# Kernel optimization log

Hardware: AMD Instinct MI355X
Metric: run time of the kernel (lower is better)

Reference implementation:

```python
import jax, jax.numpy as jnp
import numpy as np

V, E, H = 30000, 512, 512
MARGIN = 0.05


def _lstm(x, wih, whh, b):
    # x: [N,T,E]; torch LSTM gate order i,f,g,o; returns outputs [N,T,H]
    N = x.shape[0]
    Hh = whh.shape[1]
    xproj = jnp.swapaxes(x, 0, 1) @ wih.T + b  # [T,N,4H], input proj hoisted out of scan

    def step(carry, xp):
        h, c = carry
        g = xp + h @ whh.T
        i, f, gg, o = jnp.split(g, 4, axis=-1)
        c = jax.nn.sigmoid(f) * c + jax.nn.sigmoid(i) * jnp.tanh(gg)
        h = jax.nn.sigmoid(o) * jnp.tanh(c)
        return (h, c), h

    h0 = jnp.zeros((N, Hh), x.dtype)
    _, hs = jax.lax.scan(step, (h0, h0), xproj)
    return jnp.swapaxes(hs, 0, 1)


def _attn_pool(feat, lengths, aw, ab, sw, sb):
    # batched masked-softmax attention pooling (replaces per-sample python loop)
    T = feat.shape[1]
    s = (jnp.tanh(feat @ aw.T + ab) @ sw.T + sb)[..., 0]  # [N,T]
    mask = jnp.arange(T)[None, :] < lengths[:, None]
    w = jax.nn.softmax(jnp.where(mask, s, -1e30), axis=1)
    return jnp.einsum('nt,nth->nh', w, feat)  # [N,H]


def _cos(a, b, eps=1e-8):
    na = jnp.maximum(jnp.linalg.norm(a, axis=-1), eps)
    nb = jnp.maximum(jnp.linalg.norm(b, axis=-1), eps)
    return jnp.sum(a * b, axis=-1) / (na * nb)


def setup_inputs() -> dict:
    key = jax.random.key(0)
    ks = jax.random.split(key, 24)
    B, BL, T, TD = 32, 8, 128, 256
    d = {}
    d['tran'] = jax.random.randint(ks[0], (B, BL, T), 1, V)
    d['tran_len'] = jax.random.randint(ks[1], (B,), 1, T + 1)
    d['tran_block_len'] = jax.random.randint(ks[2], (B, BL), 1, T + 1)
    d['doc_anchor'] = jax.random.randint(ks[3], (B, TD), 1, V)
    d['doc_anchor_len'] = jax.random.randint(ks[4], (B,), 1, TD + 1)
    d['doc_neg'] = jax.random.randint(ks[5], (B, TD), 1, V)
    d['doc_neg_len'] = jax.random.randint(ks[6], (B,), 1, TD + 1)
    sc = 0.05
    emb = jax.random.normal(ks[7], (V, E), jnp.float32) * sc
    d['emb'] = emb.at[0].set(0.0)  # padding_idx=0
    d['tran_wih'] = jax.random.normal(ks[8], (4 * H, E), jnp.float32) * sc
    d['tran_whh'] = jax.random.normal(ks[9], (4 * H, H), jnp.float32) * sc
    d['tran_b'] = jax.random.normal(ks[10], (4 * H,), jnp.float32) * sc
    d['doc_wih'] = jax.random.normal(ks[11], (4 * H, E), jnp.float32) * sc
    d['doc_whh'] = jax.random.normal(ks[12], (4 * H, H), jnp.float32) * sc
    d['doc_b'] = jax.random.normal(ks[13], (4 * H,), jnp.float32) * sc
    d['tran_attn_w'] = jax.random.normal(ks[14], (H, H), jnp.float32) * sc
    d['tran_attn_b'] = jax.random.normal(ks[15], (H,), jnp.float32) * sc
    d['tran_s_w'] = jax.random.normal(ks[16], (1, H), jnp.float32) * sc
    d['tran_s_b'] = jax.random.normal(ks[17], (1,), jnp.float32) * sc
    d['doc_attn_w'] = jax.random.normal(ks[18], (H, H), jnp.float32) * sc
    d['doc_attn_b'] = jax.random.normal(ks[19], (H,), jnp.float32) * sc
    d['doc_s_w'] = jax.random.normal(ks[20], (1, H), jnp.float32) * sc
    d['doc_s_b'] = jax.random.normal(ks[21], (1,), jnp.float32) * sc
    return d


def reference(tran, tran_len, tran_block_len, doc_anchor, doc_anchor_len,
              doc_neg, doc_neg_len, emb, tran_wih, tran_whh, tran_b,
              doc_wih, doc_whh, doc_b, tran_attn_w, tran_attn_b,
              tran_s_w, tran_s_b, doc_attn_w, doc_attn_b, doc_s_w, doc_s_b):
    B, BL, T = tran.shape
    # --- code side: encode B*BL sub-sequences, attn pool, tanh, max over block ---
    flat = tran.reshape(B * BL, T)
    feat = _lstm(emb[flat], tran_wih, tran_whh, tran_b)  # [B*BL,T,H]
    pooled = _attn_pool(feat, tran_block_len.reshape(-1),
                        tran_attn_w, tran_attn_b, tran_s_w, tran_s_b)
    pooled = jnp.tanh(pooled)  # use_tanh on attn output (tran path)
    code_repr = jnp.max(pooled.reshape(B, BL, H), axis=1)  # max_pool over block

    # --- doc side: attn pool, no trailing tanh (doc_encoding has no use_tanh branch) ---
    def doc_enc(tok, lens):
        f = _lstm(emb[tok], doc_wih, doc_whh, doc_b)
        return _attn_pool(f, lens, doc_attn_w, doc_attn_b, doc_s_w, doc_s_b)

    da = doc_enc(doc_anchor, doc_anchor_len)
    dn = doc_enc(doc_neg, doc_neg_len)

    anchor_sim = _cos(code_repr, da)
    neg_sim = _cos(code_repr, dn)
    loss = jnp.mean(jnp.clip(MARGIN - anchor_sim + neg_sim, 1e-6, None))
    return loss
```

## Files before the change

### kernel.cpp

```cpp
#include <hip/hip_runtime.h>
#include <hip/hip_bf16.h>

#define NSEQ 320
#define NTRAN 256
#define TT 128
#define TDOC 256
#define EH 512
#define XR_TRAN (NTRAN*TT)
#define XROWS (XR_TRAN + 64*TDOC)
#define HSLOTS 6
#define FW 264

typedef __attribute__((ext_vector_type(8))) short bf16x8v;
typedef __attribute__((ext_vector_type(4))) float f32x4v;

__device__ __align__(16) unsigned short g_xb [(size_t)XROWS*EH];
__device__ __align__(16) unsigned short g_wbx[2*2048*512];
__device__ __align__(16) unsigned short g_w2b[2*5*512*512];
__device__ float g_xp[(size_t)XROWS*2048];
__device__ float g_h [HSLOTS*NSEQ*EH];
__device__ float g_sc[64*260];
__device__ float g_pool[NSEQ*EH];
__device__ float g_loss;
__device__ unsigned g_gflag[48*FW];
__device__ unsigned g_sflag[16*FW];
__device__ unsigned g_aprog[48];

__device__ __forceinline__ float sigm(float x) { return 1.0f / (1.0f + expf(-x)); }

__device__ __forceinline__ float ldg_sys(const float* p) {
  return __hip_atomic_load(p, __ATOMIC_RELAXED, __HIP_MEMORY_SCOPE_SYSTEM);
}
__device__ __forceinline__ void stg_sys(float* p, float v) {
  __hip_atomic_store(p, v, __ATOMIC_RELAXED, __HIP_MEMORY_SCOPE_SYSTEM);
}
__device__ __forceinline__ unsigned ldu(const unsigned* p) {
  return __hip_atomic_load(p, __ATOMIC_RELAXED, __HIP_MEMORY_SCOPE_AGENT);
}
__device__ __forceinline__ unsigned short f2b(float f) {
  __hip_bfloat16 h = __float2bfloat16(f);
  return *reinterpret_cast<unsigned short*>(&h);
}

__global__ __launch_bounds__(256) void init_state() {
  int i = blockIdx.x*256 + threadIdx.x;
  if (i < NSEQ*EH) g_h[5*NSEQ*EH + i] = 0.0f;
  if (i < 64*260) g_sc[i] = 0.0f;
  if (i < 48*FW) g_gflag[i] = ((i % FW) == 0) ? 4u : 0u;
  if (i < 16*FW) g_sflag[i] = 0u;
  if (i < 48) g_aprog[i] = 0u;
  if (i == 0) g_loss = 0.0f;
}

__global__ __launch_bounds__(256) void build_wbx(
    const float* __restrict__ wih_t, const float* __restrict__ wih_d) {
  int idx = blockIdx.x*256 + threadIdx.x;
  if (idx >= 2*2048*512) return;
  int p = idx / (2048*512); int rem = idx % (2048*512);
  const float* wih = p ? wih_d : wih_t;
  g_wbx[idx] = f2b(wih[rem]);
}

__global__ __launch_bounds__(256) void build_wt2(
    const float* __restrict__ whh_t, const float* __restrict__ whh_d,
    const float* __restrict__ aw_t,  const float* __restrict__ aw_d) {
  int idx = blockIdx.x*256 + threadIdx.x;
  if (idx >= 2*5*512*512) return;
  int p  = idx / (5*512*512); int rem = idx % (5*512*512);
  int cg = rem / (512*512);   int r2  = rem % (512*512);
  int k  = r2 >> 9;           int c   = r2 & 511;
  float v;
  if (cg < 4) {
    int r = (c >> 7)*512 + cg*128 + (c & 127);
    const float* whh = p ? whh_d : whh_t;
    v = whh[r*512 + k];
  } else {
    const float* aw = p ? aw_d : aw_t;
    v = aw[c*512 + k];
  }
  g_w2b[((size_t)(p*5 + cg)*512 + k)*512 + c] = f2b(v);
}

__global__ __launch_bounds__(128) void pregather(
    const int* __restrict__ tran, const int* __restrict__ da_tok,
    const int* __restrict__ dn_tok, const float* __restrict__ emb) {
  int row = blockIdx.x;
  int tok;
  if (row < XR_TRAN) tok = tran[row];
  else {
    int q = row - XR_TRAN;
    tok = (q < 32*TDOC) ? da_tok[q] : dn_tok[q - 32*TDOC];
  }
  const float4* src = (const float4*)&emb[(size_t)tok*EH];
  float4 v = src[threadIdx.x];
  uint2 o;
  o.x = (unsigned)f2b(v.x) | ((unsigned)f2b(v.y) << 16);
  o.y = (unsigned)f2b(v.z) | ((unsigned)f2b(v.w) << 16);
  ((uint2*)&g_xb[(size_t)row*EH])[threadIdx.x] = o;
}

__global__ __launch_bounds__(512, 2) void xproj_mfma(
    const float* __restrict__ b_t, const float* __restrict__ b_d) {
  __shared__ short As[2][256*32];
  __shared__ short Bs[2][256*32];
  const int bid = blockIdx.x;
  const int mt = bid >> 3, ntb = bid & 7;
  const size_t mb = (size_t)mt * 256; const int nb = ntb * 256;
  const bool tp = (mb < XR_TRAN);
  const size_t wboff = (tp ? 0 : (size_t)2048*512);
  const float* __restrict__ bias = tp ? b_t : b_d;
  const int tid = threadIdx.x;
  const int l = tid & 63, w = tid >> 6;
  const int mw = w >> 2, nw = w & 3;

  f32x4v acc[8][4];
  #pragma unroll
  for (int m2 = 0; m2 < 8; ++m2)
    #pragma unroll
    for (int n2 = 0; n2 < 4; ++n2) acc[m2][n2] = (f32x4v){0.f, 0.f, 0.f, 0.f};

  uint4 rA[2], rB[2];
  auto stage_load = [&](int k0) {
    #pragma unroll
    for (int i = 0; i < 2; ++i) {
      int u = i*512 + tid;
      rA[i] = *(const uint4*)&g_xb[(mb + (u >> 2))*512 + k0 + (u & 3)*8];
      rB[i] = *(const uint4*)&g_wbx[wboff + (size_t)(nb + (u >> 2))*512 + k0 + (u & 3)*8];
    }
  };
  auto stage_write = [&](int buf) {
    #pragma unroll
    for (int i = 0; i < 2; ++i) {
      int u = i*512 + tid;
      *(uint4*)&As[buf][u*8] = rA[i];
      *(uint4*)&Bs[buf][u*8] = rB[i];
    }
  };

  stage_load(0); stage_write(0); __syncthreads();
  for (int ks = 0; ks < 16; ++ks) {
    const int buf = ks & 1;
    if (ks < 15) stage_load((ks + 1)*32);
    bf16x8v aF[8], bF[4];
    #pragma unroll
    for (int m2 = 0; m2 < 8; ++m2)
      aF[m2] = *(const bf16x8v*)&As[buf][(mw*128 + m2*16 + (l & 15))*32 + (l >> 4)*8];
    #pragma unroll
    for (int n2 = 0; n2 < 4; ++n2)
      bF[n2] = *(const bf16x8v*)&Bs[buf][(nw*64 + n2*16 + (l & 15))*32 + (l >> 4)*8];
    #pragma unroll
    for (int m2 = 0; m2 < 8; ++m2)
      #pragma unroll
      for (int n2 = 0; n2 < 4; ++n2)
        acc[m2][n2] = __builtin_amdgcn_mfma_f32_16x16x32_bf16(aF[m2], bF[n2], acc[m2][n2], 0, 0, 0);
    __syncthreads();
    if (ks < 15) stage_write(buf ^ 1);
    __syncthreads();
  }

  #pragma unroll
  for (int n2 = 0; n2 < 4; ++n2) {
    const int colg = nb + nw*64 + n2*16 + (l & 15);
    const int col2 = ((colg & 511) >> 7)*512 + (colg >> 9)*128 + (colg & 127);
    const float bv = bias[colg];
    #pragma unroll
    for (int m2 = 0; m2 < 8; ++m2) {
      #pragma unroll
      for (int r = 0; r < 4; ++r) {
        size_t row = mb + mw*128 + m2*16 + (l >> 4)*4 + r;
        g_xp[row*2048 + col2] = acc[m2][n2][r] + bv;
      }
    }
  }
}

template<int S, int CPL>
__device__ __forceinline__ void gemm2(const unsigned short* __restrict__ wsl,
                                      const float* __restrict__ ht,
                                      float* __restrict__ part,
                                      int kq, int lane) {
  constexpr int PW = CPL*64 + 4;
  float acc[CPL][S];
  #pragma unroll
  for (int c = 0; c < CPL; ++c)
    #pragma unroll
    for (int s = 0; s < S; ++s) acc[c][s] = 0.0f;
  const unsigned short* wp = wsl + (size_t)(kq*64)*512 + CPL*lane;
  const float* hb = ht + kq*64;
  #pragma unroll 2
  for (int k4 = 0; k4 < 16; ++k4) {
    float4 hv[S];
    #pragma unroll
    for (int s = 0; s < S; ++s) hv[s] = *(const float4*)&hb[s*516 + k4*4];
    #pragma unroll
    for (int i4 = 0; i4 < 4; ++i4) {
      float wf[CPL];
      if constexpr (CPL == 8) {
        uint4 wv = *(const uint4*)(wp + (size_t)(k4*4 + i4)*512);
        wf[0] = __uint_as_float(wv.x << 16); wf[1] = __uint_as_float(wv.x & 0xFFFF0000u);
        wf[2] = __uint_as_float(wv.y << 16); wf[3] = __uint_as_float(wv.y & 0xFFFF0000u);
        wf[4] = __uint_as_float(wv.z << 16); wf[5] = __uint_as_float(wv.z & 0xFFFF0000u);
        wf[6] = __uint_as_float(wv.w << 16); wf[7] = __uint_as_float(wv.w & 0xFFFF0000u);
      } else {
        uint2 wv = *(const uint2*)(wp + (size_t)(k4*4 + i4)*512);
        wf[0] = __uint_as_float(wv.x << 16); wf[1] = __uint_as_float(wv.x & 0xFFFF0000u);
        wf[2] = __uint_as_float(wv.y << 16); wf[3] = __uint_as_float(wv.y & 0xFFFF0000u);
      }
      #pragma unroll
      for (int s = 0; s < S; ++s) {
        float h = ((const float*)&hv[s])[i4];
        #pragma unroll
        for (int c = 0; c < CPL; ++c) acc[c][s] = fmaf(wf[c], h, acc[c][s]);
      }
    }
  }
  if (kq < 4) {
    #pragma unroll
    for (int s = 0; s < S; ++s)
      #pragma unroll
      for (int c = 0; c < CPL; ++c)
        part[(size_t)(kq*S + s)*PW + CPL*lane + c] = acc[c][s];
  }
  __syncthreads();
  if (kq >= 4) {
    const int q = kq - 4;
    #pragma unroll
    for (int s = 0; s < S; ++s)
      #pragma unroll
      for (int c = 0; c < CPL; ++c)
        part[(size_t)(q*S + s)*PW + CPL*lane + c] += acc[c][s];
  }
}

__global__ __launch_bounds__(512, 2) void persist(
    const int* __restrict__ tbl, const int* __restrict__ dal, const int* __restrict__ dnl,
    const float* __restrict__ ab_t, const float* __restrict__ ab_d,
    const float* __restrict__ sw_t, const float* __restrict__ sw_d,
    const float* __restrict__ sb_t, const float* __restrict__ sb_d) {
  __shared__ float sm[28920];
  float* part = sm;
  float* ht   = sm + 16512;
  float* cb   = sm + 20640;
  float* scr  = sm + 24736;
  float* ml   = sm + 24752;
  float* lenb = sm + 24768;
  float* alb  = sm + 24776;
  float* htB  = sm + 24792;

  const int b = blockIdx.x, tid = threadIdx.x;
  const int x = b & 7, m = b >> 3;
  bool tran; int cg, nt;
  if (x < 5) { tran = true; cg = x; nt = m; }
  else { int slot = (x - 5)*32 + m; tran = false; cg = slot >> 4; nt = slot & 15; }
  const int S     = tran ? 8 : 4;
  const int Ts    = tran ? TT : TDOC;
  const int sbase = tran ? nt*8 : NTRAN + nt*4;
  const bool isattn = (cg >= 4);
  const int gr = tran ? nt : 32 + nt;
  const unsigned AK = tran ? 1u : 2u;
  const int colbase = tran ? 0 : (cg - 4) * 256;
  const int wslice  = isattn ? 4 : cg;
  const unsigned short* __restrict__ wsl =
      g_w2b + (size_t)((tran ? 0 : 5) + wslice)*512*512 + (isattn ? colbase : 0);
  const float* __restrict__ ab  = tran ? ab_t : ab_d;
  const float* __restrict__ sw  = tran ? sw_t : sw_d;
  const float  sb = tran ? sb_t[0] : sb_d[0];

  for (int i = tid; i < 4096; i += 512) cb[i] = 0.0f;
  if (tid < S) {
    ml[tid*2] = -3.0e38f; ml[tid*2+1] = 0.0f;
    int s = sbase + tid;
    int len = tran ? tbl[s] : (s < NTRAN+32 ? dal[s-NTRAN] : dnl[s-NTRAN-32]);
    lenb[tid] = (float)len;
  }
  __syncthreads();

  const int lane = tid & 63, kq = tid >> 6;
  const int w = kq;
  const int PW = tran ? 516 : (isattn ? 260 : 516);
  const int CW = isattn ? (tran ? 512 : 256) : 0;
  const int DW = isattn ? (tran ? 512 : 256) : 0;

  if (!isattn) {
    for (int t = 0; t < Ts; ++t) {
      float xpA[4], xpB[4];
      {
        int i = tid; int jl = i & 127, s = i >> 7;
        size_t row = tran ? (size_t)(sbase + s)*TT + t
                          : (size_t)XR_TRAN + (size_t)(sbase + s - NTRAN)*TDOC + t;
        const float* xr = &g_xp[row*2048 + cg*512];
        #pragma unroll
        for (int g4 = 0; g4 < 4; ++g4) xpA[g4] = xr[g4*128 + jl];
      }
      if (tran) {
        int i = tid + 512; int jl = i & 127, s = i >> 7;
        size_t row = (size_t)(sbase + s)*TT + t;
        const float* xr = &g_xp[row*2048 + cg*512];
        #pragma unroll
        for (int g4 = 0; g4 < 4; ++g4) xpB[g4] = xr[g4*128 + jl];
      }
      if (tid == 0) {
        if (t > 0)
          while (ldu(&g_gflag[gr*FW + t]) < 4u) __builtin_amdgcn_s_sleep(1);
        if (t >= 5) {
          unsigned tgt = AK * (unsigned)(t - 4);
          while (ldu(&g_aprog[gr]) < tgt) __builtin_amdgcn_s_sleep(1);
        }
      }
      __syncthreads();
      const int sp = (t + 5) % HSLOTS;
      for (int s = 0; s < S; ++s)
        ht[s*516 + kq*64 + lane] =
            ldg_sys(&g_h[((size_t)sp*NSEQ + sbase + s)*EH + kq*64 + lane]);
      if (tran) gemm2<8,8>(wsl, ht, part, kq, lane);
      else      gemm2<4,8>(wsl, ht, part, kq, lane);
      __syncthreads();
      const int so = t % HSLOTS;
      {
        int i = tid; int jl = i & 127, s = i >> 7;
        float u[4];
        #pragma unroll
        for (int g4 = 0; g4 < 4; ++g4) {
          float v = xpA[g4];
          #pragma unroll
          for (int q = 0; q < 4; ++q) v += part[(size_t)(q*S + s)*516 + g4*128 + jl];
          u[g4] = v;
        }
        float cv = cb[s*128 + jl];
        float cn = sigm(u[1])*cv + sigm(u[0])*tanhf(u[2]);
        float hn = sigm(u[3])*tanhf(cn);
        cb[s*128 + jl] = cn;
        stg_sys(&g_h[((size_t)so*NSEQ + sbase + s)*EH + cg*128 + jl], hn);
      }
      if (tran) {
        int i = tid + 512; int jl = i & 127, s = i >> 7;
        float u[4];
        #pragma unroll
        for (int g4 = 0; g4 < 4; ++g4) {
          float v = xpB[g4];
          #pragma unroll
          for (int q = 0; q < 4; ++q) v += part[(size_t)(q*S + s)*516 + g4*128 + jl];
          u[g4] = v;
        }
        float cv = cb[s*128 + jl];
        float cn = sigm(u[1])*cv + sigm(u[0])*tanhf(u[2]);
        float hn = sigm(u[3])*tanhf(cn);
        cb[s*128 + jl] = cn;
        stg_sys(&g_h[((size_t)so*NSEQ + sbase + s)*EH + cg*128 + jl], hn);
      }
      __syncthreads();
      if (tid == 0) atomicAdd(&g_gflag[gr*FW + t + 1], 1u);
    }
  } else {
    for (int t = 1; t <= Ts + 1; ++t) {
      float* hcur  = (t & 1) ? htB : ht;
      float* hprev = (t & 1) ? ht : htB;
      if (tid == 0) {
        if (t <= Ts)
          while (ldu(&g_gflag[gr*FW + t]) < 4u) __builtin_amdgcn_s_sleep(1);
        if (!tran && t >= 2)
          while (ldu(&g_sflag[nt*FW + (t - 1)]) < 2u) __builtin_amdgcn_s_sleep(1);
      }
      __syncthreads();
      const int sp = (t + 5) % HSLOTS;
      if (t <= Ts) {
        for (int s = 0; s < S; ++s)
          hcur[s*516 + kq*64 + lane] =
              ldg_sys(&g_h[((size_t)sp*NSEQ + sbase + s)*EH + kq*64 + lane]);
      }
      if (t >= 2 && tid < S) {
        int s = tid;
        if ((float)(t - 2) < lenb[s]) {
          float sv = tran ? scr[(t & 1)*8 + s]
                          : ldg_sys(&g_sc[(sbase + s - NTRAN)*260 + (t - 2)]);
          float mo = ml[s*2], lo = ml[s*2+1];
          float mn = fmaxf(mo, sv);
          float a = expf(mo - mn), e = expf(sv - mn);
          alb[s*2] = a; alb[s*2+1] = e;
          ml[s*2] = mn; ml[s*2+1] = lo*a + e;
        } else { alb[s*2] = 1.0f; alb[s*2+1] = 0.0f; }
      }
      __syncthreads();
      if (t <= Ts) {
        if (tran) gemm2<8,8>(wsl, hcur, part, kq, lane);
        else      gemm2<4,4>(wsl, hcur, part, kq, lane);
      }
      if (t >= 2) {
        for (int i = tid; i < S*DW; i += 512) {
          int s = tran ? (i >> 9) : (i >> 8);
          int dl = i & (DW - 1);
          float a = alb[s*2], e = alb[s*2+1];
          if (!(a == 1.0f && e == 0.0f)) {
            float hv = hprev[s*516 + colbase + dl];
            cb[s*DW + dl] = cb[s*DW + dl]*a + e*hv;
          }
        }
      }
      __syncthreads();
      if (tid == 0) atomicAdd(&g_aprog[gr], 1u);
      if (t <= Ts) {
        for (int i = tid; i < CW*S; i += 512) {
          int c = i & (CW - 1);
          int s = tran ? (i >> 9) : (i >> 8);
          float u = ab[colbase + c];
          #pragma unroll
          for (int q = 0; q < 4; ++q) u += part[(size_t)(q*S + s)*PW + c];
          float p = tanhf(u) * sw[colbase + c];
          part[(size_t)s*PW + c] = p;
        }
        __syncthreads();
        if (w < S) {
          int s = w;
          float p = 0.0f;
          for (int j = 0; j < CW/64; ++j) p += part[(size_t)s*PW + j*64 + lane];
          #pragma unroll
          for (int off = 32; off >= 1; off >>= 1) p += __shfl_xor(p, off, 64);
          if (lane == 0) {
            if (tran) scr[((t - 1) & 1)*8 + s] = p + sb;
            else atomicAdd(&g_sc[(sbase + s - NTRAN)*260 + (t - 1)],
                           p + (cg == 4 ? sb : 0.0f));
          }
        }
        if (!tran) {
          __syncthreads();
          if (tid == 0) atomicAdd(&g_sflag[nt*FW + t], 1u);
        }
      }
    }
    for (int i = tid; i < S*DW; i += 512) {
      int s = tran ? (i >> 9) : (i >> 8);
      int dl = i & (DW - 1);
      float v = cb[s*DW + dl] / ml[s*2+1];
      if (tran) v = tanhf(v);
      g_pool[(size_t)(sbase + s)*EH + colbase + dl] = v;
    }
  }
}

__global__ __launch_bounds__(256) void loss_partial() {
  __shared__ float red[5][4];
  int b = blockIdx.x, tid = threadIdx.x;
  float p[5] = {0.f, 0.f, 0.f, 0.f, 0.f};
  for (int j = tid; j < EH; j += 256) {
    float mx = -3.0e38f;
    #pragma unroll
    for (int bl = 0; bl < 8; bl++) mx = fmaxf(mx, g_pool[(b*8 + bl)*EH + j]);
    float da = g_pool[(NTRAN + b)*EH + j];
    float dn = g_pool[(NTRAN + 32 + b)*EH + j];
    p[0] += mx*mx; p[1] += da*da; p[2] += dn*dn; p[3] += mx*da; p[4] += mx*dn;
  }
  int lane = tid & 63, w = tid >> 6;
  #pragma unroll
  for (int i = 0; i < 5; i++) {
    float v = p[i];
    for (int off = 32; off >= 1; off >>= 1) v += __shfl_xor(v, off, 64);
    if (lane == 0) red[i][w] = v;
  }
  __syncthreads();
  if (tid == 0) {
    float cc = red[0][0]+red[0][1]+red[0][2]+red[0][3];
    float aa = red[1][0]+red[1][1]+red[1][2]+red[1][3];
    float nn = red[2][0]+red[2][1]+red[2][2]+red[2][3];
    float ca = red[3][0]+red[3][1]+red[3][2]+red[3][3];
    float cn = red[4][0]+red[4][1]+red[4][2]+red[4][3];
    float ncr = fmaxf(sqrtf(cc), 1e-8f);
    float nda = fmaxf(sqrtf(aa), 1e-8f);
    float ndn = fmaxf(sqrtf(nn), 1e-8f);
    float simA = ca / (ncr * nda);
    float simN = cn / (ncr * ndn);
    float term = fmaxf(0.05f - simA + simN, 1e-6f);
    atomicAdd(&g_loss, term * (1.0f / 32.0f));
  }
}

__global__ void write_out(float* __restrict__ out) {
  if (threadIdx.x == 0 && blockIdx.x == 0) out[0] = g_loss;
}

extern "C" void kernel_launch(void* const* d_in, const int* in_sizes, int n_in,
                              void* d_out, int out_size, void* d_ws, size_t ws_size,
                              hipStream_t stream) {
  (void)in_sizes; (void)n_in; (void)out_size; (void)d_ws; (void)ws_size;
  const int*   tran   = (const int*)d_in[0];
  const int*   tbl    = (const int*)d_in[2];
  const int*   da_tok = (const int*)d_in[3];
  const int*   dal    = (const int*)d_in[4];
  const int*   dn_tok = (const int*)d_in[5];
  const int*   dnl    = (const int*)d_in[6];
  const float* emb    = (const float*)d_in[7];
  const float* wih_t  = (const float*)d_in[8];
  const float* whh_t  = (const float*)d_in[9];
  const float* b_t    = (const float*)d_in[10];
  const float* wih_d  = (const float*)d_in[11];
  const float* whh_d  = (const float*)d_in[12];
  const float* b_d    = (const float*)d_in[13];
  const float* aw_t   = (const float*)d_in[14];
  const float* ab_t   = (const float*)d_in[15];
  const float* sw_t   = (const float*)d_in[16];
  const float* sb_t   = (const float*)d_in[17];
  const float* aw_d   = (const float*)d_in[18];
  const float* ab_d   = (const float*)d_in[19];
  const float* sw_d   = (const float*)d_in[20];
  const float* sb_d   = (const float*)d_in[21];

  init_state<<<(NSEQ*EH + 255)/256, 256, 0, stream>>>();
  build_wbx<<<(2*2048*512 + 255)/256, 256, 0, stream>>>(wih_t, wih_d);
  build_wt2<<<(2*5*512*512 + 255)/256, 256, 0, stream>>>(whh_t, whh_d, aw_t, aw_d);
  pregather<<<XROWS, 128, 0, stream>>>(tran, da_tok, dn_tok, emb);
  xproj_mfma<<<(XROWS/256)*8, 512, 0, stream>>>(b_t, b_d);

  persist<<<256, 512, 0, stream>>>(tbl, dal, dnl,
      ab_t, ab_d, sw_t, sw_d, sb_t, sb_d);

  loss_partial<<<32, 256, 0, stream>>>();
  write_out<<<1, 64, 0, stream>>>((float*)d_out);
}
```

Measured before the change: 2.991 ms.

## Repartition doc LSTM blocks into 8-sequence groups with split gate columns

Doc-side work is re-split so each group covers 8 sequences instead of 4. Each gate block now handles half of a 128-column gate group (64 columns, CPL=4), and each attention block handles a 128-column quarter (CPL=2). The aim is to give the doc recurrence, which is the longer critical path at 256 steps, more column parallelism per step and to match the 8-sequence batching of the tran path. The cost is more blocks per group to synchronise: flag targets rise to 8 gate blocks and 4 attention blocks, which adds atomic traffic. The initial t=0 flag seeding is removed, relying on the t>0 guard.

```diff
diff --git a/kernel.cpp b/kernel.cpp
--- a/kernel.cpp
+++ b/kernel.cpp
@@ -46,7 +46,7 @@
   int i = blockIdx.x*256 + threadIdx.x;
   if (i < NSEQ*EH) g_h[5*NSEQ*EH + i] = 0.0f;
   if (i < 64*260) g_sc[i] = 0.0f;
-  if (i < 48*FW) g_gflag[i] = ((i % FW) == 0) ? 4u : 0u;
+  if (i < 48*FW) g_gflag[i] = 0u;
   if (i < 16*FW) g_sflag[i] = 0u;
   if (i < 48) g_aprog[i] = 0u;
   if (i == 0) g_loss = 0.0f;
@@ -175,17 +175,17 @@
 }
 
 template<int S, int CPL>
-__device__ __forceinline__ void gemm2(const unsigned short* __restrict__ wsl,
+__device__ __forceinline__ void gemm2(const unsigned short* __restrict__ wpl,
                                       const float* __restrict__ ht,
                                       float* __restrict__ part,
-                                      int kq, int lane) {
+                                      int kq, int clbase) {
   constexpr int PW = CPL*64 + 4;
   float acc[CPL][S];
   #pragma unroll
   for (int c = 0; c < CPL; ++c)
     #pragma unroll
     for (int s = 0; s < S; ++s) acc[c][s] = 0.0f;
-  const unsigned short* wp = wsl + (size_t)(kq*64)*512 + CPL*lane;
+  const unsigned short* wp = wpl + (size_t)(kq*64)*512;
   const float* hb = ht + kq*64;
   #pragma unroll 2
   for (int k4 = 0; k4 < 16; ++k4) {
@@ -201,10 +201,13 @@
         wf[2] = __uint_as_float(wv.y << 16); wf[3] = __uint_as_float(wv.y & 0xFFFF0000u);
         wf[4] = __uint_as_float(wv.z << 16); wf[5] = __uint_as_float(wv.z & 0xFFFF0000u);
         wf[6] = __uint_as_float(wv.w << 16); wf[7] = __uint_as_float(wv.w & 0xFFFF0000u);
-      } else {
+      } else if constexpr (CPL == 4) {
         uint2 wv = *(const uint2*)(wp + (size_t)(k4*4 + i4)*512);
         wf[0] = __uint_as_float(wv.x << 16); wf[1] = __uint_as_float(wv.x & 0xFFFF0000u);
         wf[2] = __uint_as_float(wv.y << 16); wf[3] = __uint_as_float(wv.y & 0xFFFF0000u);
+      } else {
+        unsigned wv = *(const unsigned*)(wp + (size_t)(k4*4 + i4)*512);
+        wf[0] = __uint_as_float(wv << 16); wf[1] = __uint_as_float(wv & 0xFFFF0000u);
       }
       #pragma unroll
       for (int s = 0; s < S; ++s) {
@@ -219,7 +222,7 @@
     for (int s = 0; s < S; ++s)
       #pragma unroll
       for (int c = 0; c < CPL; ++c)
-        part[(size_t)(kq*S + s)*PW + CPL*lane + c] = acc[c][s];
+        part[(size_t)(kq*S + s)*PW + clbase + c] = acc[c][s];
   }
   __syncthreads();
   if (kq >= 4) {
@@ -228,7 +231,7 @@
     for (int s = 0; s < S; ++s)
       #pragma unroll
       for (int c = 0; c < CPL; ++c)
-        part[(size_t)(q*S + s)*PW + CPL*lane + c] += acc[c][s];
+        part[(size_t)(q*S + s)*PW + clbase + c] += acc[c][s];
   }
 }
 
@@ -249,22 +252,37 @@
 
   const int b = blockIdx.x, tid = threadIdx.x;
   const int x = b & 7, m = b >> 3;
-  bool tran; int cg, nt;
-  if (x < 5) { tran = true; cg = x; nt = m; }
-  else { int slot = (x - 5)*32 + m; tran = false; cg = slot >> 4; nt = slot & 15; }
-  const int S     = tran ? 8 : 4;
-  const int Ts    = tran ? TT : TDOC;
-  const int sbase = tran ? nt*8 : NTRAN + nt*4;
-  const bool isattn = (cg >= 4);
-  const int gr = tran ? nt : 32 + nt;
-  const unsigned AK = tran ? 1u : 2u;
-  const int colbase = tran ? 0 : (cg - 4) * 256;
-  const int wslice  = isattn ? 4 : cg;
-  const unsigned short* __restrict__ wsl =
-      g_w2b + (size_t)((tran ? 0 : 5) + wslice)*512*512 + (isattn ? colbase : 0);
-  const float* __restrict__ ab  = tran ? ab_t : ab_d;
-  const float* __restrict__ sw  = tran ? sw_t : sw_d;
+  const bool tran = (x < 5);
+  const int S = 8;
+  int gr, sbase, Ts, grd = 0, cgx = 0, halfx = 0, q4 = 0;
+  bool isattn;
+  unsigned GN, AK;
+  if (tran) {
+    gr = m; sbase = m*8; Ts = TT; GN = 4u; AK = 1u;
+    isattn = (x == 4); cgx = x;
+  } else {
+    int slot = (x - 5)*32 + m; grd = slot / 12; int role = slot % 12;
+    gr = 32 + grd; sbase = NTRAN + grd*8; Ts = TDOC; GN = 8u; AK = 4u;
+    isattn = (role >= 8);
+    if (!isattn) { cgx = role >> 1; halfx = role & 1; } else { q4 = role - 8; }
+  }
+  const int wslice = tran ? (isattn ? 4 : cgx) : (5 + (isattn ? 4 : cgx));
+  const unsigned short* __restrict__ wbase = g_w2b + (size_t)wslice*512*512;
+  const float* __restrict__ ab = tran ? ab_t : ab_d;
+  const float* __restrict__ sw = tran ? sw_t : sw_d;
   const float  sb = tran ? sb_t[0] : sb_d[0];
+
+  const int lane = tid & 63, kq = tid >> 6;
+  const int w = kq;
+  int coloff, clbase;
+  if (tran)            { coloff = lane*8;                                    clbase = lane*8; }
+  else if (!isattn)    { coloff = (lane>>4)*128 + halfx*64 + (lane&15)*4;    clbase = (lane>>4)*64 + (lane&15)*4; }
+  else                 { coloff = q4*128 + lane*2;                           clbase = lane*2; }
+  const unsigned short* __restrict__ wpl = wbase + coloff;
+  const int PW = tran ? 516 : (isattn ? 132 : 260);
+  const int CW = isattn ? (tran ? 512 : 128) : 0;
+  const int DW = CW;
+  const int colbase = isattn ? (tran ? 0 : q4*128) : 0;
 
   for (int i = tid; i < 4096; i += 512) cb[i] = 0.0f;
   if (tid < S) {
@@ -275,33 +293,30 @@
   }
   __syncthreads();
 
-  const int lane = tid & 63, kq = tid >> 6;
-  const int w = kq;
-  const int PW = tran ? 516 : (isattn ? 260 : 516);
-  const int CW = isattn ? (tran ? 512 : 256) : 0;
-  const int DW = isattn ? (tran ? 512 : 256) : 0;
-
   if (!isattn) {
     for (int t = 0; t < Ts; ++t) {
       float xpA[4], xpB[4];
-      {
-        int i = tid; int jl = i & 127, s = i >> 7;
-        size_t row = tran ? (size_t)(sbase + s)*TT + t
-                          : (size_t)XR_TRAN + (size_t)(sbase + s - NTRAN)*TDOC + t;
-        const float* xr = &g_xp[row*2048 + cg*512];
+      if (tran) {
+        { int i = tid; int jl = i & 127, s = i >> 7;
+          size_t row = (size_t)(sbase + s)*TT + t;
+          const float* xr = &g_xp[row*2048 + cgx*512];
+          #pragma unroll
+          for (int g4 = 0; g4 < 4; ++g4) xpA[g4] = xr[g4*128 + jl]; }
+        { int i = tid + 512; int jl = i & 127, s = i >> 7;
+          size_t row = (size_t)(sbase + s)*TT + t;
+          const float* xr = &g_xp[row*2048 + cgx*512];
+          #pragma unroll
+          for (int g4 = 0; g4 < 4; ++g4) xpB[g4] = xr[g4*128 + jl]; }
+      } else {
+        int jl = tid & 63, s = tid >> 6;
+        size_t row = (size_t)XR_TRAN + (size_t)(sbase + s - NTRAN)*TDOC + t;
+        const float* xr = &g_xp[row*2048 + cgx*512 + halfx*64];
         #pragma unroll
         for (int g4 = 0; g4 < 4; ++g4) xpA[g4] = xr[g4*128 + jl];
       }
-      if (tran) {
-        int i = tid + 512; int jl = i & 127, s = i >> 7;
-        size_t row = (size_t)(sbase + s)*TT + t;
-        const float* xr = &g_xp[row*2048 + cg*512];
-        #pragma unroll
-        for (int g4 = 0; g4 < 4; ++g4) xpB[g4] = xr[g4*128 + jl];
-      }
       if (tid == 0) {
         if (t > 0)
-          while (ldu(&g_gflag[gr*FW + t]) < 4u) __builtin_amdgcn_s_sleep(1);
+          while (ldu(&g_gflag[gr*FW + t]) < GN) __builtin_amdgcn_s_sleep(1);
         if (t >= 5) {
           unsigned tgt = AK * (unsigned)(t - 4);
           while (ldu(&g_aprog[gr]) < tgt) __builtin_amdgcn_s_sleep(1);
@@ -312,41 +327,43 @@
       for (int s = 0; s < S; ++s)
         ht[s*516 + kq*64 + lane] =
             ldg_sys(&g_h[((size_t)sp*NSEQ + sbase + s)*EH + kq*64 + lane]);
-      if (tran) gemm2<8,8>(wsl, ht, part, kq, lane);
-      else      gemm2<4,8>(wsl, ht, part, kq, lane);
+      if (tran) gemm2<8,8>(wpl, ht, part, kq, clbase);
+      else      gemm2<8,4>(wpl, ht, part, kq, clbase);
       __syncthreads();
       const int so = t % HSLOTS;
-      {
-        int i = tid; int jl = i & 127, s = i >> 7;
+      if (tran) {
+        #pragma unroll
+        for (int ch2 = 0; ch2 < 2; ++ch2) {
+          int i = tid + ch2*512; int jl = i & 127, s = i >> 7;
+          float u[4];
+          #pragma unroll
+          for (int g4 = 0; g4 < 4; ++g4) {
+            float v = ch2 ? xpB[g4] : xpA[g4];
+            #pragma unroll
+            for (int q = 0; q < 4; ++q) v += part[(size_t)(q*S + s)*516 + g4*128 + jl];
+            u[g4] = v;
+          }
+          float cv = cb[s*128 + jl];
+          float cn = sigm(u[1])*cv + sigm(u[0])*tanhf(u[2]);
+          float hn = sigm(u[3])*tanhf(cn);
+          cb[s*128 + jl] = cn;
+          stg_sys(&g_h[((size_t)so*NSEQ + sbase + s)*EH + cgx*128 + jl], hn);
+        }
+      } else {
+        int jl = tid & 63, s = tid >> 6;
         float u[4];
         #pragma unroll
         for (int g4 = 0; g4 < 4; ++g4) {
           float v = xpA[g4];
           #pragma unroll
-          for (int q = 0; q < 4; ++q) v += part[(size_t)(q*S + s)*516 + g4*128 + jl];
+          for (int q = 0; q < 4; ++q) v += part[(size_t)(q*S + s)*260 + g4*64 + jl];
           u[g4] = v;
         }
-        float cv = cb[s*128 + jl];
+        float cv = cb[s*64 + jl];
         float cn = sigm(u[1])*cv + sigm(u[0])*tanhf(u[2]);
         float hn = sigm(u[3])*tanhf(cn);
-        cb[s*128 + jl] = cn;
-        stg_sys(&g_h[((size_t)so*NSEQ + sbase + s)*EH + cg*128 + jl], hn);
-      }
-      if (tran) {
-        int i = tid + 512; int jl = i & 127, s = i >> 7;
-        float u[4];
-        #pragma unroll
-        for (int g4 = 0; g4 < 4; ++g4) {
-          float v = xpB[g4];
-          #pragma unroll
-          for (int q = 0; q < 4; ++q) v += part[(size_t)(q*S + s)*516 + g4*128 + jl];
-          u[g4] = v;
-        }
-        float cv = cb[s*128 + jl];
-        float cn = sigm(u[1])*cv + sigm(u[0])*tanhf(u[2]);
-        float hn = sigm(u[3])*tanhf(cn);
-        cb[s*128 + jl] = cn;
-        stg_sys(&g_h[((size_t)so*NSEQ + sbase + s)*EH + cg*128 + jl], hn);
+        cb[s*64 + jl] = cn;
+        stg_sys(&g_h[((size_t)so*NSEQ + sbase + s)*EH + cgx*128 + halfx*64 + jl], hn);
       }
       __syncthreads();
       if (tid == 0) atomicAdd(&g_gflag[gr*FW + t + 1], 1u);
@@ -357,9 +374,9 @@
       float* hprev = (t & 1) ? ht : htB;
       if (tid == 0) {
         if (t <= Ts)
-          while (ldu(&g_gflag[gr*FW + t]) < 4u) __builtin_amdgcn_s_sleep(1);
+          while (ldu(&g_gflag[gr*FW + t]) < GN) __builtin_amdgcn_s_sleep(1);
         if (!tran && t >= 2)
-          while (ldu(&g_sflag[nt*FW + (t - 1)]) < 2u) __builtin_amdgcn_s_sleep(1);
+          while (ldu(&g_sflag[grd*FW + (t - 1)]) < 4u) __builtin_amdgcn_s_sleep(1);
       }
       __syncthreads();
       const int sp = (t + 5) % HSLOTS;
@@ -382,12 +399,12 @@
       }
       __syncthreads();
       if (t <= Ts) {
-        if (tran) gemm2<8,8>(wsl, hcur, part, kq, lane);
-        else      gemm2<4,4>(wsl, hcur, part, kq, lane);
+        if (tran) gemm2<8,8>(wpl, hcur, part, kq, clbase);
+        else      gemm2<8,2>(wpl, hcur, part, kq, clbase);
       }
       if (t >= 2) {
         for (int i = tid; i < S*DW; i += 512) {
-          int s = tran ? (i >> 9) : (i >> 8);
+          int s = tran ? (i >> 9) : (i >> 7);
           int dl = i & (DW - 1);
           float a = alb[s*2], e = alb[s*2+1];
           if (!(a == 1.0f && e == 0.0f)) {
@@ -401,7 +418,7 @@
       if (t <= Ts) {
         for (int i = tid; i < CW*S; i += 512) {
           int c = i & (CW - 1);
-          int s = tran ? (i >> 9) : (i >> 8);
+          int s = tran ? (i >> 9) : (i >> 7);
           float u = ab[colbase + c];
           #pragma unroll
           for (int q = 0; q < 4; ++q) u += part[(size_t)(q*S + s)*PW + c];
@@ -418,17 +435,17 @@
           if (lane == 0) {
             if (tran) scr[((t - 1) & 1)*8 + s] = p + sb;
             else atomicAdd(&g_sc[(sbase + s - NTRAN)*260 + (t - 1)],
-                           p + (cg == 4 ? sb : 0.0f));
+                           p + (q4 == 0 ? sb : 0.0f));
           }
         }
         if (!tran) {
           __syncthreads();
-          if (tid == 0) atomicAdd(&g_sflag[nt*FW + t], 1u);
+          if (tid == 0) atomicAdd(&g_sflag[grd*FW + t], 1u);
         }
       }
     }
     for (int i = tid; i < S*DW; i += 512) {
-      int s = tran ? (i >> 9) : (i >> 8);
+      int s = tran ? (i >> 9) : (i >> 7);
       int dl = i & (DW - 1);
       float v = cb[s*DW + dl] / ml[s*2+1];
       if (tran) v = tanhf(v);
```

Measured after the change: 3.401 ms. 1.14x slower.
